# Performance work log

Hardware: AMD Instinct MI355X
Metric: run time of the kernel (lower is better)

Reference implementation:

```python
import jax, jax.numpy as jnp
import numpy as np

DIM, ORDER, HID = 512, 2, 64
B, S = 4, 8192


def setup_inputs() -> dict:
    key = jax.random.key(0)
    ks = jax.random.split(key, 16)
    rnd = lambda k, shape, scale: (jax.random.normal(k, shape, dtype=jnp.float32) * scale)
    return {
        'x': rnd(ks[0], (B, S, DIM), 1.0),
        # ImplicitFilter MLP: Linear(1,64) -> GELU -> Linear(64,64) -> GELU -> Linear(64,dim)
        'w1': rnd(ks[1], (1, HID), 1.0),
        'b1': rnd(ks[2], (HID,), 0.02),
        'w2': rnd(ks[3], (HID, HID), 1.0 / np.sqrt(HID)),
        'b2': rnd(ks[4], (HID,), 0.02),
        'w3': rnd(ks[5], (HID, DIM), 1.0 / np.sqrt(HID)),
        'b3': rnd(ks[6], (DIM,), 0.02),
        # depthwise Conv1d(dim, dim, k=3, padding=1, groups=dim): weight (dim, 3)
        'conv_w': rnd(ks[7], (DIM, 3), 1.0 / np.sqrt(3)),
        'conv_b': rnd(ks[8], (DIM,), 0.02),
        # in_proj: Linear(dim, dim*(order+1))
        'w_in': rnd(ks[9], (DIM, DIM * (ORDER + 1)), 1.0 / np.sqrt(DIM)),
        'b_in': rnd(ks[10], (DIM * (ORDER + 1),), 0.02),
        # out_proj: Linear(dim, dim)
        'w_out': rnd(ks[11], (DIM, DIM), 1.0 / np.sqrt(DIM)),
        'b_out': rnd(ks[12], (DIM,), 0.02),
    }


def _gelu(x):
    return jax.nn.gelu(x, approximate=False)  # torch nn.GELU default is exact erf


def reference(x, w1, b1, w2, b2, w3, b3, conv_w, conv_b, w_in, b_in, w_out, b_out):
    batch, seq_len, dim = x.shape
    # in_proj and split into order+1 paths
    proj = x @ w_in + b_in                      # (B, S, 3D)
    v, u, z = jnp.split(proj, 3, axis=-1)       # each (B, S, D)
    # implicit filter from positions
    pos = jnp.linspace(0.0, 1.0, seq_len, dtype=x.dtype)[:, None]   # (S, 1)
    filt = _gelu(_gelu(pos @ w1 + b1) @ w2 + b2) @ w3 + b3          # (S, D)
    # depthwise short conv, kernel=3, padding=1 (cross-correlation as in torch)
    up = jnp.pad(u, ((0, 0), (1, 1), (0, 0)))
    u_short = (up[:, :-2] * conv_w[:, 0] + up[:, 1:-1] * conv_w[:, 1]
               + up[:, 2:] * conv_w[:, 2] + conv_b)                 # (B, S, D)
    # FFT long convolution (circular, matching torch rfft/irfft with n=seq_len)
    U = jnp.fft.rfft(u_short, axis=1)                               # (B, S//2+1, D)
    F = jnp.fft.rfft(filt, n=seq_len, axis=0)[None]                 # (1, S//2+1, D)
    filtered = jnp.fft.irfft(U * F, n=seq_len, axis=1)              # (B, S, D)
    # multiplicative gates
    out = v * filtered * jax.nn.sigmoid(z)
    return out @ w_out + b_out
```

## Files before the change

### kernel.cpp

```cpp
#include <hip/hip_runtime.h>
#include <math.h>

#define DIM   512
#define NB    4
#define NS    8192
#define FFT_N 8192
#define FT    1024
#define MTOT  (NB*NS)

typedef __attribute__((ext_vector_type(8))) short bf16x8;
typedef __attribute__((ext_vector_type(4))) short short4v;
typedef __attribute__((ext_vector_type(8))) short short8v;
typedef __attribute__((ext_vector_type(4))) float f32x4;

__device__ __forceinline__ float bf2f(unsigned short u) {
    union { unsigned int i; float f; } v; v.i = ((unsigned int)u) << 16; return v.f;
}
__device__ __forceinline__ unsigned short f2bf(float f) {
    union { float f; unsigned int i; } v; v.f = f;
    unsigned int r = v.i + 0x7fffu + ((v.i >> 16) & 1u);
    return (unsigned short)(r >> 16);
}
__device__ __forceinline__ float2 cmulf(float2 a, float2 b) {
    return make_float2(a.x*b.x - a.y*b.y, a.x*b.y + a.y*b.x);
}
__device__ __forceinline__ float2 cadd(float2 a, float2 b) { return make_float2(a.x+b.x, a.y+b.y); }
__device__ __forceinline__ float2 csub(float2 a, float2 b) { return make_float2(a.x-b.x, a.y-b.y); }
__device__ __forceinline__ float gelu_exact(float x) {
    return 0.5f * x * (1.0f + erff(x * 0.70710678118654752f));
}
__device__ __forceinline__ void gload16(const void* g, void* l) {
    __builtin_amdgcn_global_load_lds((const __attribute__((address_space(1))) void*)g,
                                     (__attribute__((address_space(3))) void*)l, 16, 0, 0);
}

__global__ void filter_mlp_kernel(const float* __restrict__ w1, const float* __restrict__ b1,
                                  const float* __restrict__ w2, const float* __restrict__ b2,
                                  const float* __restrict__ w3, const float* __restrict__ b3,
                                  float* __restrict__ filt) {
    __shared__ float h1[64];
    __shared__ float h2[64];
    const int s = blockIdx.x;
    const int t = threadIdx.x;
    const float pos = (float)s / (float)(NS - 1);
    h1[t] = gelu_exact(pos * w1[t] + b1[t]);
    __syncthreads();
    float acc = b2[t];
    #pragma unroll 8
    for (int j = 0; j < 64; ++j) acc += h1[j] * w2[j*64 + t];
    h2[t] = gelu_exact(acc);
    __syncthreads();
    for (int d = t; d < DIM; d += 64) {
        float o = b3[d];
        #pragma unroll 8
        for (int j = 0; j < 64; ++j) o += h2[j] * w3[j*DIM + d];
        filt[(size_t)s*DIM + d] = o;
    }
}

__global__ void transpose_f32_kernel(const float* __restrict__ in, float* __restrict__ out,
                                     int R, int C) {
    __shared__ float tile[64][65];
    const int c0 = blockIdx.x * 64, r0 = blockIdx.y * 64;
    const int t = threadIdx.x;
    const int rr = t >> 4, c4 = (t & 15) * 4;
    #pragma unroll
    for (int p = 0; p < 4; ++p) {
        const int r = rr + p*16;
        float4 v = *(const float4*)&in[(size_t)(r0 + r)*C + c0 + c4];
        tile[r][c4+0]=v.x; tile[r][c4+1]=v.y; tile[r][c4+2]=v.z; tile[r][c4+3]=v.w;
    }
    __syncthreads();
    const int cc = t >> 4, r4 = (t & 15) * 4;
    #pragma unroll
    for (int p = 0; p < 4; ++p) {
        const int c = cc + p*16;
        float4 o = make_float4(tile[r4+0][c], tile[r4+1][c], tile[r4+2][c], tile[r4+3][c]);
        *(float4*)&out[(size_t)(c0 + c)*R + r0 + r4] = o;
    }
}

__global__ void castT_kernel(const float* __restrict__ in, unsigned short* __restrict__ outT,
                             int R, int C) {
    __shared__ float tile[64][65];
    const int c0 = blockIdx.x * 64, r0 = blockIdx.y * 64;
    const int t = threadIdx.x;
    const int rr = t >> 4, c4 = (t & 15) * 4;
    #pragma unroll
    for (int p = 0; p < 4; ++p) {
        const int r = rr + p*16;
        float4 v = *(const float4*)&in[(size_t)(r0 + r)*C + c0 + c4];
        tile[r][c4+0]=v.x; tile[r][c4+1]=v.y; tile[r][c4+2]=v.z; tile[r][c4+3]=v.w;
    }
    __syncthreads();
    const int cc = t >> 4, r4 = (t & 15) * 4;
    #pragma unroll
    for (int p = 0; p < 4; ++p) {
        const int c = cc + p*16;
        short4v o;
        o[0] = (short)f2bf(tile[r4+0][c]); o[1] = (short)f2bf(tile[r4+1][c]);
        o[2] = (short)f2bf(tile[r4+2][c]); o[3] = (short)f2bf(tile[r4+3][c]);
        *(short4v*)&outT[(size_t)(c0 + c)*R + r0 + r4] = o;
    }
}

__global__ void cast_x_kernel(const float* __restrict__ in, unsigned short* __restrict__ out) {
    const size_t i = ((size_t)blockIdx.x * 256 + threadIdx.x) * 8;
    float4 a = *(const float4*)&in[i];
    float4 b = *(const float4*)&in[i+4];
    short8v o;
    o[0]=(short)f2bf(a.x); o[1]=(short)f2bf(a.y); o[2]=(short)f2bf(a.z); o[3]=(short)f2bf(a.w);
    o[4]=(short)f2bf(b.x); o[5]=(short)f2bf(b.y); o[6]=(short)f2bf(b.z); o[7]=(short)f2bf(b.w);
    *(short8v*)&out[i] = o;
}

template<int LOGQ>
__device__ __forceinline__ void dif4_stage(float2* X) {
    const int q = 1 << LOGQ;
    const float step = -6.28318530717958647692f / (float)(4*q);
    #pragma unroll
    for (int it = 0; it < (FFT_N/4)/FT; ++it) {
        const int idx = threadIdx.x + it*FT;
        const int g = idx >> LOGQ, k = idx & (q-1);
        const int base = (g << (LOGQ+2)) + k;
        float2 a=X[base], b=X[base+q], c=X[base+2*q], d=X[base+3*q];
        float2 t0=cadd(a,c), t1=csub(a,c), t2=cadd(b,d), t3=csub(b,d);
        float2 y0=cadd(t0,t2), y2=csub(t0,t2);
        float2 y1=make_float2(t1.x+t3.y, t1.y-t3.x);
        float2 y3=make_float2(t1.x-t3.y, t1.y+t3.x);
        float sv, cv; __sincosf(step*(float)k, &sv, &cv);
        float2 w1=make_float2(cv, sv);
        float2 w2=cmulf(w1, w1);
        float2 w3=cmulf(w2, w1);
        X[base]     = y0;
        X[base+q]   = cmulf(y1, w1);
        X[base+2*q] = cmulf(y2, w2);
        X[base+3*q] = cmulf(y3, w3);
    }
    __syncthreads();
}

template<int LOGQ>
__device__ __forceinline__ void dit4_stage_inv(float2* X) {
    const int q = 1 << LOGQ;
    const float step = 6.28318530717958647692f / (float)(4*q);
    #pragma unroll
    for (int it = 0; it < (FFT_N/4)/FT; ++it) {
        const int idx = threadIdx.x + it*FT;
        const int g = idx >> LOGQ, k = idx & (q-1);
        const int base = (g << (LOGQ+2)) + k;
        float sv, cv; __sincosf(step*(float)k, &sv, &cv);
        float2 w1=make_float2(cv, sv);
        float2 w2=cmulf(w1, w1);
        float2 w3=cmulf(w2, w1);
        float2 u0=X[base];
        float2 u1=cmulf(X[base+q],   w1);
        float2 u2=cmulf(X[base+2*q], w2);
        float2 u3=cmulf(X[base+3*q], w3);
        float2 s02=cadd(u0,u2), d02=csub(u0,u2);
        float2 s13=cadd(u1,u3), d13=csub(u1,u3);
        X[base]     = cadd(s02, s13);
        X[base+2*q] = csub(s02, s13);
        X[base+q]   = make_float2(d02.x - d13.y, d02.y + d13.x);
        X[base+3*q] = make_float2(d02.x + d13.y, d02.y - d13.x);
    }
    __syncthreads();
}

__device__ __forceinline__ void reg_fwd(float2* E) {
    const float C = 0.70710678118654752f;
    {
        float2 t0=cadd(E[0],E[4]), t1=csub(E[0],E[4]);
        float2 t2=cadd(E[2],E[6]), t3=csub(E[2],E[6]);
        E[0]=cadd(t0,t2);
        E[4]=csub(t0,t2);
        E[2]=make_float2(t1.x+t3.y, t1.y-t3.x);
        E[6]=make_float2(t1.x-t3.y, t1.y+t3.x);
    }
    {
        float2 t0=cadd(E[1],E[5]), t1=csub(E[1],E[5]);
        float2 t2=cadd(E[3],E[7]), t3=csub(E[3],E[7]);
        float2 y0=cadd(t0,t2), y2=csub(t0,t2);
        float2 y1=make_float2(t1.x+t3.y, t1.y-t3.x);
        float2 y3=make_float2(t1.x-t3.y, t1.y+t3.x);
        E[1]=y0;
        E[3]=make_float2(C*(y1.x+y1.y),  C*(y1.y-y1.x));
        E[5]=make_float2(y2.y, -y2.x);
        E[7]=make_float2(C*(y3.y-y3.x), -C*(y3.x+y3.y));
    }
    #pragma unroll
    for (int j = 0; j < 8; j += 2) {
        float2 a=E[j], b=E[j+1];
        E[j]=cadd(a,b); E[j+1]=csub(a,b);
    }
}
__device__ __forceinline__ void reg_inv(float2* E) {
    const float C = 0.70710678118654752f;
    #pragma unroll
    for (int j = 0; j < 8; j += 2) {
        float2 a=E[j], b=E[j+1];
        E[j]=cadd(a,b); E[j+1]=csub(a,b);
    }
    {
        float2 u0=E[0], u1=E[2], u2=E[4], u3=E[6];
        float2 s02=cadd(u0,u2), d02=csub(u0,u2);
        float2 s13=cadd(u1,u3), d13=csub(u1,u3);
        E[0]=cadd(s02,s13);
        E[4]=csub(s02,s13);
        E[2]=make_float2(d02.x - d13.y, d02.y + d13.x);
        E[6]=make_float2(d02.x + d13.y, d02.y - d13.x);
    }
    {
        float2 z1=E[3], z2=E[5], z3=E[7];
        float2 u0=E[1];
        float2 u1=make_float2(C*(z1.x - z1.y), C*(z1.x + z1.y));
        float2 u2=make_float2(-z2.y, z2.x);
        float2 u3=make_float2(-C*(z3.x + z3.y), C*(z3.x - z3.y));
        float2 s02=cadd(u0,u2), d02=csub(u0,u2);
        float2 s13=cadd(u1,u3), d13=csub(u1,u3);
        E[1]=cadd(s02,s13);
        E[5]=csub(s02,s13);
        E[3]=make_float2(d02.x - d13.y, d02.y + d13.x);
        E[7]=make_float2(d02.x + d13.y, d02.y - d13.x);
    }
}

__device__ __forceinline__ void load8(const float2* X, int t, float2* E) {
    const float4* b = (const float4*)(X + 8*t);
    #pragma unroll
    for (int p = 0; p < 4; ++p) {
        float4 v = b[p];
        E[2*p]   = make_float2(v.x, v.y);
        E[2*p+1] = make_float2(v.z, v.w);
    }
}
__device__ __forceinline__ void store8(float2* X, int t, const float2* E) {
    float4* b = (float4*)(X + 8*t);
    #pragma unroll
    for (int p = 0; p < 4; ++p)
        b[p] = make_float4(E[2*p].x, E[2*p].y, E[2*p+1].x, E[2*p+1].y);
}

__global__ __launch_bounds__(FT)
void fft_filt_kernel(const float* __restrict__ filtT, float2* __restrict__ Fbr) {
    extern __shared__ float4 Xraw[];
    float2* X = (float2*)Xraw;
    const int dd = blockIdx.x;
    const int t = threadIdx.x;
    const float* f = filtT + (size_t)dd * FFT_N;
    {
        float4 a = *(const float4*)(f + 8*t);
        float4 b = *(const float4*)(f + 8*t + 4);
        float2 E[8];
        E[0]=make_float2(a.x,0.f); E[1]=make_float2(a.y,0.f);
        E[2]=make_float2(a.z,0.f); E[3]=make_float2(a.w,0.f);
        E[4]=make_float2(b.x,0.f); E[5]=make_float2(b.y,0.f);
        E[6]=make_float2(b.z,0.f); E[7]=make_float2(b.w,0.f);
        store8(X, t, E);
    }
    __syncthreads();
    dif4_stage<11>(X);
    dif4_stage<9>(X);
    dif4_stage<7>(X);
    dif4_stage<5>(X);
    dif4_stage<3>(X);
    {
        float2 E[8];
        load8(X, t, E);
        reg_fwd(E);
        float2* o = Fbr + (size_t)dd*FFT_N + 8*t;
        #pragma unroll
        for (int j = 0; j < 8; ++j) o[j] = E[j];
    }
}

__global__ __launch_bounds__(FT)
void fft_conv_kernel(unsigned short* __restrict__ uT, const float2* __restrict__ Fbr) {
    extern __shared__ float4 Xraw[];
    float2* X = (float2*)Xraw;
    const int d = blockIdx.x & (DIM - 1);
    const int p = blockIdx.x >> 9;
    unsigned short* u1 = uT + (size_t)((2*p    )*DIM + d) * FFT_N;
    unsigned short* u2 = uT + (size_t)((2*p + 1)*DIM + d) * FFT_N;
    const int t = threadIdx.x;
    {
        short8v a = *(const short8v*)(u1 + 8*t);
        short8v b = *(const short8v*)(u2 + 8*t);
        float2 E[8];
        #pragma unroll
        for (int j = 0; j < 8; ++j)
            E[j] = make_float2(bf2f((unsigned short)a[j]), bf2f((unsigned short)b[j]));
        store8(X, t, E);
    }
    __syncthreads();
    dif4_stage<11>(X);
    dif4_stage<9>(X);
    dif4_stage<7>(X);
    dif4_stage<5>(X);
    dif4_stage<3>(X);
    {
        float2 E[8];
        load8(X, t, E);
        reg_fwd(E);
        const float2* F = Fbr + (size_t)d*FFT_N + 8*t;
        #pragma unroll
        for (int j = 0; j < 8; ++j) E[j] = cmulf(E[j], F[j]);
        reg_inv(E);
        store8(X, t, E);
    }
    __syncthreads();
    dit4_stage_inv<3>(X);
    dit4_stage_inv<5>(X);
    dit4_stage_inv<7>(X);
    dit4_stage_inv<9>(X);
    dit4_stage_inv<11>(X);
    {
        float2 E[8];
        load8(X, t, E);
        const float sc = 1.0f / (float)FFT_N;
        short8v a, b;
        #pragma unroll
        for (int j = 0; j < 8; ++j) {
            a[j] = (short)f2bf(E[j].x * sc);
            b[j] = (short)f2bf(E[j].y * sc);
        }
        *(short8v*)(u1 + 8*t) = a;
        *(short8v*)(u2 + 8*t) = b;
    }
}

__global__ void conv_transpose_kernel(const unsigned short* __restrict__ u,
                                      const float* __restrict__ conv_w,
                                      const float* __restrict__ conv_b,
                                      unsigned short* __restrict__ uT) {
    __shared__ float tile[66][65];
    const int bid = blockIdx.x;
    const int dt = bid & 7, st = (bid >> 3) & 127, b = bid >> 10;
    const int d0 = dt*64, s0 = st*64;
    const int t = threadIdx.x;
    const int rr = t >> 4, c4 = (t & 15) * 4;
    for (int r = rr; r < 66; r += 16) {
        const int s = s0 + r - 1;
        float v0=0.f, v1=0.f, v2=0.f, v3=0.f;
        if (s >= 0 && s < NS) {
            short4v xv = *(const short4v*)&u[((size_t)(b*NS + s))*DIM + d0 + c4];
            v0=bf2f((unsigned short)xv[0]); v1=bf2f((unsigned short)xv[1]);
            v2=bf2f((unsigned short)xv[2]); v3=bf2f((unsigned short)xv[3]);
        }
        tile[r][c4]=v0; tile[r][c4+1]=v1; tile[r][c4+2]=v2; tile[r][c4+3]=v3;
    }
    __syncthreads();
    const int dl = t >> 4, s4 = (t & 15) * 4;
    #pragma unroll
    for (int p = 0; p < 4; ++p) {
        const int dc = dl + p*16;
        const int d = d0 + dc;
        const float w0 = conv_w[d*3], w1 = conv_w[d*3+1], w2 = conv_w[d*3+2];
        const float cb = conv_b[d];
        short4v o;
        #pragma unroll
        for (int j = 0; j < 4; ++j) {
            const int sx = s4 + j;
            const float val = tile[sx][dc]*w0 + tile[sx+1][dc]*w1 + tile[sx+2][dc]*w2 + cb;
            o[j] = (short)f2bf(val);
        }
        *(short4v*)&uT[((size_t)(b*DIM + d))*FFT_N + s0 + s4] = o;
    }
}

__global__ void gate_kernel(unsigned short* __restrict__ vg, const unsigned short* __restrict__ yT) {
    __shared__ float tile[64][65];
    const int bid = blockIdx.x;
    const int dt = bid & 7, st = (bid >> 3) & 127, b = bid >> 10;
    const int d0 = dt*64, s0 = st*64;
    const int t = threadIdx.x;
    const int dl = t >> 4, s4 = (t & 15) * 4;
    #pragma unroll
    for (int p = 0; p < 4; ++p) {
        const int d = dl + p*16;
        short4v y = *(const short4v*)&yT[((size_t)(b*DIM + d0 + d))*FFT_N + s0 + s4];
        tile[d][s4]  =bf2f((unsigned short)y[0]); tile[d][s4+1]=bf2f((unsigned short)y[1]);
        tile[d][s4+2]=bf2f((unsigned short)y[2]); tile[d][s4+3]=bf2f((unsigned short)y[3]);
    }
    __syncthreads();
    const int sl = t >> 4, d4 = (t & 15) * 4;
    #pragma unroll
    for (int p = 0; p < 4; ++p) {
        const int s = s0 + sl + p*16;
        unsigned short* pv = &vg[((size_t)(b*NS + s))*DIM + d0 + d4];
        short4v v = *(short4v*)pv;
        short4v o;
        #pragma unroll
        for (int j = 0; j < 4; ++j)
            o[j] = (short)f2bf(bf2f((unsigned short)v[j]) * tile[d4+j][sl + p*16]);
        *(short4v*)pv = o;
    }
}

template<int MODE>
__global__ __launch_bounds__(256)
void gemm_bt_kernel(const unsigned short* __restrict__ A,
                    const unsigned short* __restrict__ BT,
                    const float* __restrict__ bias,
                    float* __restrict__ Cf,
                    unsigned short* __restrict__ Cb) {
    __shared__ unsigned short As[2][4096];
    __shared__ unsigned short Bs[2][4096];
    const int tid = threadIdx.x;
    const int wid = tid >> 6, lane = tid & 63;
    const int bid = blockIdx.y * 4 + blockIdx.x;
    const int swz = (bid & 7) * 128 + (bid >> 3);
    const int m0 = (swz >> 2) * 128, n0 = (swz & 3) * 128;
    const int srow = wid*16 + (lane >> 2);
    const int scol = (lane & 3) * 8;
    const unsigned short* gA = A  + (size_t)(m0 + srow)*DIM + scol;
    const unsigned short* gB = BT + (size_t)(n0 + srow)*DIM + scol;
    const int wr = wid >> 1, wc = wid & 1;
    const int fr = lane & 15, fq = lane >> 4;
    f32x4 acc[4][4] = {};
    gload16(gA,                  &As[0][wid*512]);
    gload16(gA + (size_t)64*DIM, &As[0][wid*512 + 2048]);
    gload16(gB,                  &Bs[0][wid*512]);
    gload16(gB + (size_t)64*DIM, &Bs[0][wid*512 + 2048]);
    int cur = 0;
    for (int k0 = 0; k0 < DIM; k0 += 32) {
        __syncthreads();
        if (k0 + 32 < DIM) {
            const int nx = cur ^ 1;
            gload16(gA + k0 + 32,                  &As[nx][wid*512]);
            gload16(gA + k0 + 32 + (size_t)64*DIM, &As[nx][wid*512 + 2048]);
            gload16(gB + k0 + 32,                  &Bs[nx][wid*512]);
            gload16(gB + k0 + 32 + (size_t)64*DIM, &Bs[nx][wid*512 + 2048]);
        }
        bf16x8 af[4], bfr[4];
        #pragma unroll
        for (int mi = 0; mi < 4; ++mi)
            af[mi] = *(const bf16x8*)&As[cur][(wr*64 + mi*16 + fr)*32 + fq*8];
        #pragma unroll
        for (int ni = 0; ni < 4; ++ni)
            bfr[ni] = *(const bf16x8*)&Bs[cur][(wc*64 + ni*16 + fr)*32 + fq*8];
        #pragma unroll
        for (int mi = 0; mi < 4; ++mi)
            #pragma unroll
            for (int ni = 0; ni < 4; ++ni)
                acc[mi][ni] = __builtin_amdgcn_mfma_f32_16x16x32_bf16(af[mi], bfr[ni], acc[mi][ni], 0, 0, 0);
        cur ^= 1;
    }
    #pragma unroll
    for (int ni = 0; ni < 4; ++ni) {
        const int c = n0 + wc*64 + ni*16 + fr;
        const float bv = bias[c];
        #pragma unroll
        for (int mi = 0; mi < 4; ++mi) {
            const int rbase = m0 + wr*64 + mi*16 + fq*4;
            #pragma unroll
            for (int j = 0; j < 4; ++j) {
                const size_t idx = (size_t)(rbase + j)*DIM + c;
                const float val = acc[mi][ni][j] + bv;
                if (MODE == 0) Cb[idx] = f2bf(val);
                else           Cf[idx] = val;
            }
        }
    }
}

__global__ __launch_bounds__(256)
void gemm_vz_kernel(const unsigned short* __restrict__ A,
                    const unsigned short* __restrict__ BT,
                    const float* __restrict__ bias,
                    unsigned short* __restrict__ Cb) {
    __shared__ unsigned short As[2][4096];
    __shared__ unsigned short Bv[2][4096];
    __shared__ unsigned short Bz[2][4096];
    const int tid = threadIdx.x;
    const int wid = tid >> 6, lane = tid & 63;
    const int bid = blockIdx.y * 4 + blockIdx.x;
    const int swz = (bid & 7) * 128 + (bid >> 3);
    const int m0 = (swz >> 2) * 128, n0 = (swz & 3) * 128;
    const int srow = wid*16 + (lane >> 2);
    const int scol = (lane & 3) * 8;
    const unsigned short* gA  = A  + (size_t)(m0 + srow)*DIM + scol;
    const unsigned short* gBv = BT + (size_t)(n0 + srow)*DIM + scol;
    const unsigned short* gBz = BT + (size_t)(1024 + n0 + srow)*DIM + scol;
    const int wr = wid >> 1, wc = wid & 1;
    const int fr = lane & 15, fq = lane >> 4;
    f32x4 accv[4][4] = {};
    f32x4 accz[4][4] = {};
    gload16(gA,                   &As[0][wid*512]);
    gload16(gA  + (size_t)64*DIM, &As[0][wid*512 + 2048]);
    gload16(gBv,                  &Bv[0][wid*512]);
    gload16(gBv + (size_t)64*DIM, &Bv[0][wid*512 + 2048]);
    gload16(gBz,                  &Bz[0][wid*512]);
    gload16(gBz + (size_t)64*DIM, &Bz[0][wid*512 + 2048]);
    int cur = 0;
    for (int k0 = 0; k0 < DIM; k0 += 32) {
        __syncthreads();
        if (k0 + 32 < DIM) {
            const int nx = cur ^ 1;
            gload16(gA  + k0 + 32,                  &As[nx][wid*512]);
            gload16(gA  + k0 + 32 + (size_t)64*DIM, &As[nx][wid*512 + 2048]);
            gload16(gBv + k0 + 32,                  &Bv[nx][wid*512]);
            gload16(gBv + k0 + 32 + (size_t)64*DIM, &Bv[nx][wid*512 + 2048]);
            gload16(gBz + k0 + 32,                  &Bz[nx][wid*512]);
            gload16(gBz + k0 + 32 + (size_t)64*DIM, &Bz[nx][wid*512 + 2048]);
        }
        bf16x8 af[4], bf_[4];
        #pragma unroll
        for (int mi = 0; mi < 4; ++mi)
            af[mi] = *(const bf16x8*)&As[cur][(wr*64 + mi*16 + fr)*32 + fq*8];
        #pragma unroll
        for (int ni = 0; ni < 4; ++ni)
            bf_[ni] = *(const bf16x8*)&Bv[cur][(wc*64 + ni*16 + fr)*32 + fq*8];
        #pragma unroll
        for (int mi = 0; mi < 4; ++mi)
            #pragma unroll
            for (int ni = 0; ni < 4; ++ni)
                accv[mi][ni] = __builtin_amdgcn_mfma_f32_16x16x32_bf16(af[mi], bf_[ni], accv[mi][ni], 0, 0, 0);
        #pragma unroll
        for (int ni = 0; ni < 4; ++ni)
            bf_[ni] = *(const bf16x8*)&Bz[cur][(wc*64 + ni*16 + fr)*32 + fq*8];
        #pragma unroll
        for (int mi = 0; mi < 4; ++mi)
            #pragma unroll
            for (int ni = 0; ni < 4; ++ni)
                accz[mi][ni] = __builtin_amdgcn_mfma_f32_16x16x32_bf16(af[mi], bf_[ni], accz[mi][ni], 0, 0, 0);
        cur ^= 1;
    }
    #pragma unroll
    for (int ni = 0; ni < 4; ++ni) {
        const int c = n0 + wc*64 + ni*16 + fr;
        const float bv = bias[c];
        const float bz = bias[1024 + c];
        #pragma unroll
        for (int mi = 0; mi < 4; ++mi) {
            const int rbase = m0 + wr*64 + mi*16 + fq*4;
            #pragma unroll
            for (int j = 0; j < 4; ++j) {
                const size_t idx = (size_t)(rbase + j)*DIM + c;
                const float vv = accv[mi][ni][j] + bv;
                const float zz = accz[mi][ni][j] + bz;
                const float sg = 1.0f / (1.0f + __expf(-zz));
                Cb[idx] = f2bf(vv * sg);
            }
        }
    }
}

extern "C" void kernel_launch(void* const* d_in, const int* in_sizes, int n_in,
                              void* d_out, int out_size, void* d_ws, size_t ws_size,
                              hipStream_t stream) {
    const float* x      = (const float*)d_in[0];
    const float* w1     = (const float*)d_in[1];
    const float* b1     = (const float*)d_in[2];
    const float* w2     = (const float*)d_in[3];
    const float* b2     = (const float*)d_in[4];
    const float* w3     = (const float*)d_in[5];
    const float* b3     = (const float*)d_in[6];
    const float* conv_w = (const float*)d_in[7];
    const float* conv_b = (const float*)d_in[8];
    const float* w_in   = (const float*)d_in[9];
    const float* b_in   = (const float*)d_in[10];
    const float* w_out  = (const float*)d_in[11];
    const float* b_out  = (const float*)d_in[12];
    float* out = (float*)d_out;

    const size_t NEED = 167772160ULL;
    if (ws_size < NEED) return;
    char* ws = (char*)d_ws;
    float2*         Fbr    = (float2*)ws;
    unsigned short* xb     = (unsigned short*)(ws + (size_t)( 32<<20));
    unsigned short* W2     = (unsigned short*)(ws + (size_t)( 64<<20));
    unsigned short* W3     = (unsigned short*)(ws + (size_t)( 96<<20));
    char*           W4     = ws + (size_t)(128<<20);
    float*          filt   = (float*)W4;
    float*          filtT  = (float*)(ws + (size_t)(96<<20));
    unsigned short* w_inT  = (unsigned short*)W4;
    unsigned short* w_outT = (unsigned short*)(W4 + (size_t)(2<<20));

    filter_mlp_kernel<<<NS, 64, 0, stream>>>(w1, b1, w2, b2, w3, b3, filt);
    transpose_f32_kernel<<<dim3(DIM/64, NS/64), 256, 0, stream>>>(filt, filtT, NS, DIM);
    fft_filt_kernel<<<DIM, FT, FFT_N*sizeof(float2), stream>>>(filtT, Fbr);
    cast_x_kernel<<<(MTOT*DIM/8)/256, 256, 0, stream>>>(x, xb);
    castT_kernel<<<dim3(1536/64, DIM/64), 256, 0, stream>>>(w_in, w_inT, DIM, 1536);
    castT_kernel<<<dim3(DIM/64, DIM/64), 256, 0, stream>>>(w_out, w_outT, DIM, DIM);
    gemm_bt_kernel<0><<<dim3(4, MTOT/128), 256, 0, stream>>>(xb, w_inT + 512*DIM, b_in + 512, nullptr, W2);
    conv_transpose_kernel<<<NB*(NS/64)*(DIM/64), 256, 0, stream>>>(W2, conv_w, conv_b, W3);
    fft_conv_kernel<<<(NB/2)*DIM, FT, FFT_N*sizeof(float2), stream>>>(W3, Fbr);
    gemm_vz_kernel<<<dim3(4, MTOT/128), 256, 0, stream>>>(xb, w_inT, b_in, W2);
    gate_kernel<<<NB*(NS/64)*(DIM/64), 256, 0, stream>>>(W2, W3);
    gemm_bt_kernel<2><<<dim3(4, MTOT/128), 256, 0, stream>>>(W2, w_outT, b_out, out, nullptr);
}
```

Baseline: 259.1 us.

## Pad FFT shared memory against bank conflicts and fuse gate into v/z GEMM

Two changes. First, the FFT kernels now use a statically sized shared array with one padding element every 8 complex values (IDX macro, 9-stride load/store), so the radix-4 stages and per-thread 8-element accesses hit fewer LDS bank conflicts. Second, the separate gate kernel is removed: the v/z GEMM epilogue reads the FFT-filtered result directly from the transposed buffer and multiplies it in, which saves a full read/write pass over a B*S*D bf16 tensor and one launch. In exchange, the padded layout gives up 16-byte vector LDS accesses in favor of 8-byte ones, and the epilogue's reads of the transposed buffer are strided.

```diff
diff --git a/kernel.cpp b/kernel.cpp
--- a/kernel.cpp
+++ b/kernel.cpp
@@ -7,6 +7,9 @@
 #define FFT_N 8192
 #define FT    1024
 #define MTOT  (NB*NS)
+
+#define IDX(i) ((i) + ((i) >> 3))
+#define XSZ   9216
 
 typedef __attribute__((ext_vector_type(8))) short bf16x8;
 typedef __attribute__((ext_vector_type(4))) short short4v;
@@ -123,7 +126,8 @@
         const int idx = threadIdx.x + it*FT;
         const int g = idx >> LOGQ, k = idx & (q-1);
         const int base = (g << (LOGQ+2)) + k;
-        float2 a=X[base], b=X[base+q], c=X[base+2*q], d=X[base+3*q];
+        const int i0 = IDX(base), i1 = IDX(base+q), i2 = IDX(base+2*q), i3 = IDX(base+3*q);
+        float2 a=X[i0], b=X[i1], c=X[i2], d=X[i3];
         float2 t0=cadd(a,c), t1=csub(a,c), t2=cadd(b,d), t3=csub(b,d);
         float2 y0=cadd(t0,t2), y2=csub(t0,t2);
         float2 y1=make_float2(t1.x+t3.y, t1.y-t3.x);
@@ -132,10 +136,10 @@
         float2 w1=make_float2(cv, sv);
         float2 w2=cmulf(w1, w1);
         float2 w3=cmulf(w2, w1);
-        X[base]     = y0;
-        X[base+q]   = cmulf(y1, w1);
-        X[base+2*q] = cmulf(y2, w2);
-        X[base+3*q] = cmulf(y3, w3);
+        X[i0] = y0;
+        X[i1] = cmulf(y1, w1);
+        X[i2] = cmulf(y2, w2);
+        X[i3] = cmulf(y3, w3);
     }
     __syncthreads();
 }
@@ -149,20 +153,21 @@
         const int idx = threadIdx.x + it*FT;
         const int g = idx >> LOGQ, k = idx & (q-1);
         const int base = (g << (LOGQ+2)) + k;
+        const int i0 = IDX(base), i1 = IDX(base+q), i2 = IDX(base+2*q), i3 = IDX(base+3*q);
         float sv, cv; __sincosf(step*(float)k, &sv, &cv);
         float2 w1=make_float2(cv, sv);
         float2 w2=cmulf(w1, w1);
         float2 w3=cmulf(w2, w1);
-        float2 u0=X[base];
-        float2 u1=cmulf(X[base+q],   w1);
-        float2 u2=cmulf(X[base+2*q], w2);
-        float2 u3=cmulf(X[base+3*q], w3);
+        float2 u0=X[i0];
+        float2 u1=cmulf(X[i1], w1);
+        float2 u2=cmulf(X[i2], w2);
+        float2 u3=cmulf(X[i3], w3);
         float2 s02=cadd(u0,u2), d02=csub(u0,u2);
         float2 s13=cadd(u1,u3), d13=csub(u1,u3);
-        X[base]     = cadd(s02, s13);
-        X[base+2*q] = csub(s02, s13);
-        X[base+q]   = make_float2(d02.x - d13.y, d02.y + d13.x);
-        X[base+3*q] = make_float2(d02.x + d13.y, d02.y - d13.x);
+        X[i0] = cadd(s02, s13);
+        X[i2] = csub(s02, s13);
+        X[i1] = make_float2(d02.x - d13.y, d02.y + d13.x);
+        X[i3] = make_float2(d02.x + d13.y, d02.y - d13.x);
     }
     __syncthreads();
 }
@@ -225,26 +230,20 @@
     }
 }
 
-__device__ __forceinline__ void load8(const float2* X, int t, float2* E) {
-    const float4* b = (const float4*)(X + 8*t);
-    #pragma unroll
-    for (int p = 0; p < 4; ++p) {
-        float4 v = b[p];
-        E[2*p]   = make_float2(v.x, v.y);
-        E[2*p+1] = make_float2(v.z, v.w);
-    }
-}
-__device__ __forceinline__ void store8(float2* X, int t, const float2* E) {
-    float4* b = (float4*)(X + 8*t);
-    #pragma unroll
-    for (int p = 0; p < 4; ++p)
-        b[p] = make_float4(E[2*p].x, E[2*p].y, E[2*p+1].x, E[2*p+1].y);
+__device__ __forceinline__ void load8p(const float2* X, int t, float2* E) {
+    const float2* b = X + 9*t;
+    #pragma unroll
+    for (int j = 0; j < 8; ++j) E[j] = b[j];
+}
+__device__ __forceinline__ void store8p(float2* X, int t, const float2* E) {
+    float2* b = X + 9*t;
+    #pragma unroll
+    for (int j = 0; j < 8; ++j) b[j] = E[j];
 }
 
 __global__ __launch_bounds__(FT)
 void fft_filt_kernel(const float* __restrict__ filtT, float2* __restrict__ Fbr) {
-    extern __shared__ float4 Xraw[];
-    float2* X = (float2*)Xraw;
+    __shared__ float2 X[XSZ];
     const int dd = blockIdx.x;
     const int t = threadIdx.x;
     const float* f = filtT + (size_t)dd * FFT_N;
@@ -256,7 +255,7 @@
         E[2]=make_float2(a.z,0.f); E[3]=make_float2(a.w,0.f);
         E[4]=make_float2(b.x,0.f); E[5]=make_float2(b.y,0.f);
         E[6]=make_float2(b.z,0.f); E[7]=make_float2(b.w,0.f);
-        store8(X, t, E);
+        store8p(X, t, E);
     }
     __syncthreads();
     dif4_stage<11>(X);
@@ -266,7 +265,7 @@
     dif4_stage<3>(X);
     {
         float2 E[8];
-        load8(X, t, E);
+        load8p(X, t, E);
         reg_fwd(E);
         float2* o = Fbr + (size_t)dd*FFT_N + 8*t;
         #pragma unroll
@@ -276,8 +275,7 @@
 
 __global__ __launch_bounds__(FT)
 void fft_conv_kernel(unsigned short* __restrict__ uT, const float2* __restrict__ Fbr) {
-    extern __shared__ float4 Xraw[];
-    float2* X = (float2*)Xraw;
+    __shared__ float2 X[XSZ];
     const int d = blockIdx.x & (DIM - 1);
     const int p = blockIdx.x >> 9;
     unsigned short* u1 = uT + (size_t)((2*p    )*DIM + d) * FFT_N;
@@ -290,7 +288,7 @@
         #pragma unroll
         for (int j = 0; j < 8; ++j)
             E[j] = make_float2(bf2f((unsigned short)a[j]), bf2f((unsigned short)b[j]));
-        store8(X, t, E);
+        store8p(X, t, E);
     }
     __syncthreads();
     dif4_stage<11>(X);
@@ -300,13 +298,13 @@
     dif4_stage<3>(X);
     {
         float2 E[8];
-        load8(X, t, E);
+        load8p(X, t, E);
         reg_fwd(E);
         const float2* F = Fbr + (size_t)d*FFT_N + 8*t;
         #pragma unroll
         for (int j = 0; j < 8; ++j) E[j] = cmulf(E[j], F[j]);
         reg_inv(E);
-        store8(X, t, E);
+        store8p(X, t, E);
     }
     __syncthreads();
     dit4_stage_inv<3>(X);
@@ -316,7 +314,7 @@
     dit4_stage_inv<11>(X);
     {
         float2 E[8];
-        load8(X, t, E);
+        load8p(X, t, E);
         const float sc = 1.0f / (float)FFT_N;
         short8v a, b;
         #pragma unroll
@@ -365,35 +363,6 @@
             o[j] = (short)f2bf(val);
         }
         *(short4v*)&uT[((size_t)(b*DIM + d))*FFT_N + s0 + s4] = o;
-    }
-}
-
-__global__ void gate_kernel(unsigned short* __restrict__ vg, const unsigned short* __restrict__ yT) {
-    __shared__ float tile[64][65];
-    const int bid = blockIdx.x;
-    const int dt = bid & 7, st = (bid >> 3) & 127, b = bid >> 10;
-    const int d0 = dt*64, s0 = st*64;
-    const int t = threadIdx.x;
-    const int dl = t >> 4, s4 = (t & 15) * 4;
-    #pragma unroll
-    for (int p = 0; p < 4; ++p) {
-        const int d = dl + p*16;
-        short4v y = *(const short4v*)&yT[((size_t)(b*DIM + d0 + d))*FFT_N + s0 + s4];
-        tile[d][s4]  =bf2f((unsigned short)y[0]); tile[d][s4+1]=bf2f((unsigned short)y[1]);
-        tile[d][s4+2]=bf2f((unsigned short)y[2]); tile[d][s4+3]=bf2f((unsigned short)y[3]);
-    }
-    __syncthreads();
-    const int sl = t >> 4, d4 = (t & 15) * 4;
-    #pragma unroll
-    for (int p = 0; p < 4; ++p) {
-        const int s = s0 + sl + p*16;
-        unsigned short* pv = &vg[((size_t)(b*NS + s))*DIM + d0 + d4];
-        short4v v = *(short4v*)pv;
-        short4v o;
-        #pragma unroll
-        for (int j = 0; j < 4; ++j)
-            o[j] = (short)f2bf(bf2f((unsigned short)v[j]) * tile[d4+j][sl + p*16]);
-        *(short4v*)pv = o;
     }
 }
 
@@ -465,10 +434,11 @@
 }
 
 __global__ __launch_bounds__(256)
-void gemm_vz_kernel(const unsigned short* __restrict__ A,
-                    const unsigned short* __restrict__ BT,
-                    const float* __restrict__ bias,
-                    unsigned short* __restrict__ Cb) {
+void gemm_vzg_kernel(const unsigned short* __restrict__ A,
+                     const unsigned short* __restrict__ BT,
+                     const float* __restrict__ bias,
+                     const unsigned short* __restrict__ yT,
+                     unsigned short* __restrict__ Cb) {
     __shared__ unsigned short As[2][4096];
     __shared__ unsigned short Bv[2][4096];
     __shared__ unsigned short Bz[2][4096];
@@ -526,13 +496,17 @@
                 accz[mi][ni] = __builtin_amdgcn_mfma_f32_16x16x32_bf16(af[mi], bf_[ni], accz[mi][ni], 0, 0, 0);
         cur ^= 1;
     }
+    const int b    = m0 >> 13;
+    const int srel = (m0 & (NS-1)) + wr*64;
     #pragma unroll
     for (int ni = 0; ni < 4; ++ni) {
         const int c = n0 + wc*64 + ni*16 + fr;
         const float bv = bias[c];
         const float bz = bias[1024 + c];
+        const unsigned short* yrow = yT + ((size_t)(b*DIM + c))*FFT_N + srel;
         #pragma unroll
         for (int mi = 0; mi < 4; ++mi) {
+            const short4v yv = *(const short4v*)&yrow[mi*16 + fq*4];
             const int rbase = m0 + wr*64 + mi*16 + fq*4;
             #pragma unroll
             for (int j = 0; j < 4; ++j) {
@@ -540,7 +514,8 @@
                 const float vv = accv[mi][ni][j] + bv;
                 const float zz = accz[mi][ni][j] + bz;
                 const float sg = 1.0f / (1.0f + __expf(-zz));
-                Cb[idx] = f2bf(vv * sg);
+                const float yf = bf2f((unsigned short)yv[j]);
+                Cb[idx] = f2bf(vv * sg * yf);
             }
         }
     }
@@ -579,14 +554,13 @@
 
     filter_mlp_kernel<<<NS, 64, 0, stream>>>(w1, b1, w2, b2, w3, b3, filt);
     transpose_f32_kernel<<<dim3(DIM/64, NS/64), 256, 0, stream>>>(filt, filtT, NS, DIM);
-    fft_filt_kernel<<<DIM, FT, FFT_N*sizeof(float2), stream>>>(filtT, Fbr);
+    fft_filt_kernel<<<DIM, FT, 0, stream>>>(filtT, Fbr);
     cast_x_kernel<<<(MTOT*DIM/8)/256, 256, 0, stream>>>(x, xb);
     castT_kernel<<<dim3(1536/64, DIM/64), 256, 0, stream>>>(w_in, w_inT, DIM, 1536);
     castT_kernel<<<dim3(DIM/64, DIM/64), 256, 0, stream>>>(w_out, w_outT, DIM, DIM);
     gemm_bt_kernel<0><<<dim3(4, MTOT/128), 256, 0, stream>>>(xb, w_inT + 512*DIM, b_in + 512, nullptr, W2);
     conv_transpose_kernel<<<NB*(NS/64)*(DIM/64), 256, 0, stream>>>(W2, conv_w, conv_b, W3);
-    fft_conv_kernel<<<(NB/2)*DIM, FT, FFT_N*sizeof(float2), stream>>>(W3, Fbr);
-    gemm_vz_kernel<<<dim3(4, MTOT/128), 256, 0, stream>>>(xb, w_inT, b_in, W2);
-    gate_kernel<<<NB*(NS/64)*(DIM/64), 256, 0, stream>>>(W2, W3);
+    fft_conv_kernel<<<(NB/2)*DIM, FT, 0, stream>>>(W3, Fbr);
+    gemm_vzg_kernel<<<dim3(4, MTOT/128), 256, 0, stream>>>(xb, w_inT, b_in, W3, W2);
     gemm_bt_kernel<2><<<dim3(4, MTOT/128), 256, 0, stream>>>(W2, w_outT, b_out, out, nullptr);
 }
```

After: 269.1 us. 1.04x slower.
